# Kernel optimization log

Measured on AMD Instinct MI355X. Metric: run time of the kernel, lower is better.

## Reference

```python
import jax, jax.numpy as jnp
import numpy as np

BN_EPS = 1e-5


def _bn(x, gamma, beta):
    # BatchNorm2d in training mode: batch statistics over (B, T, V) per channel.
    mean = jnp.mean(x, axis=(0, 2, 3), keepdims=True)
    var = jnp.var(x, axis=(0, 2, 3), keepdims=True)
    inv = jax.lax.rsqrt(var + BN_EPS)
    g = gamma[None, :, None, None]
    b = beta[None, :, None, None]
    return (x - mean) * inv * g + b


def setup_inputs() -> dict:
    key = jax.random.key(0)
    ks = jax.random.split(key, 8)
    B, Cin, Cout, T, V = 32, 64, 128, 300, 25
    x = jax.random.normal(ks[0], (B, Cin, T, V), dtype=jnp.float32)
    A_hat = jax.random.uniform(ks[1], (V, V), dtype=jnp.float32) / V  # row-normalized-ish adjacency
    # spatial 1x1 conv weight/bias
    w_sp = jax.random.normal(ks[2], (Cout, Cin), dtype=jnp.float32) * (1.0 / np.sqrt(Cin))
    b_sp = jnp.zeros((Cout,), dtype=jnp.float32)
    g_sp = jnp.ones((Cout,), dtype=jnp.float32)
    be_sp = jnp.zeros((Cout,), dtype=jnp.float32)
    # temporal conv (9,1) weight/bias, same channels
    w_t = jax.random.normal(ks[3], (Cout, Cout, 9, 1), dtype=jnp.float32) * (1.0 / np.sqrt(Cout * 9))
    b_t = jnp.zeros((Cout,), dtype=jnp.float32)
    g_t = jnp.ones((Cout,), dtype=jnp.float32)
    be_t = jnp.zeros((Cout,), dtype=jnp.float32)
    # residual 1x1 conv + BN (in_channels != out_channels)
    w_r = jax.random.normal(ks[4], (Cout, Cin), dtype=jnp.float32) * (1.0 / np.sqrt(Cin))
    b_r = jnp.zeros((Cout,), dtype=jnp.float32)
    g_r = jnp.ones((Cout,), dtype=jnp.float32)
    be_r = jnp.zeros((Cout,), dtype=jnp.float32)
    return {
        "x": x, "A_hat": A_hat,
        "w_sp": w_sp, "b_sp": b_sp, "g_sp": g_sp, "be_sp": be_sp,
        "w_t": w_t, "b_t": b_t, "g_t": g_t, "be_t": be_t,
        "w_r": w_r, "b_r": b_r, "g_r": g_r, "be_r": be_r,
    }


def reference(x, A_hat, w_sp, b_sp, g_sp, be_sp, w_t, b_t, g_t, be_t, w_r, b_r, g_r, be_r):
    # residual branch: 1x1 conv + BN
    res = jnp.einsum('oc,bctv->botv', w_r, x) + b_r[None, :, None, None]
    res = _bn(res, g_r, be_r)
    # spatial graph conv: A_hat @ x over node dim, then 1x1 conv
    h = jnp.einsum('vw,bctw->bctv', A_hat, x)
    h = jnp.einsum('oc,bctv->botv', w_sp, h) + b_sp[None, :, None, None]
    h = jax.nn.relu(_bn(h, g_sp, be_sp))
    # temporal conv (9,1) with padding (4,0), then BN
    h = jax.lax.conv_general_dilated(
        h, w_t, window_strides=(1, 1), padding=((4, 4), (0, 0)),
        dimension_numbers=('NCHW', 'OIHW', 'NCHW'))
    h = h + b_t[None, :, None, None]
    h = _bn(h, g_t, be_t)
    return jax.nn.relu(h + res)
```

## Files before the change

### kernel.cpp

```cpp
#include <hip/hip_runtime.h>

constexpr int B    = 32;
constexpr int CIN  = 64;
constexpr int COUT = 128;
constexpr int T    = 300;
constexpr int V    = 25;
constexpr int TV   = T * V;
constexpr long long NPC   = (long long)B * TV;
constexpr long long TOTAL = (long long)B * COUT * TV;

typedef short          bf16x8 __attribute__((ext_vector_type(8)));
typedef float          f32x4  __attribute__((ext_vector_type(4)));
typedef unsigned short us8    __attribute__((ext_vector_type(8)));
typedef unsigned short us4    __attribute__((ext_vector_type(4)));

static __device__ __forceinline__ unsigned short f2bf(float f) {
  union { float f; unsigned u; } x; x.f = f;
  unsigned r = x.u + 0x7FFFu + ((x.u >> 16) & 1u);
  return (unsigned short)(r >> 16);
}
static __device__ __forceinline__ float bf2f(unsigned short u) {
  union { unsigned u; float f; } x; x.u = ((unsigned)u) << 16;
  return x.f;
}
static __device__ __forceinline__ unsigned cvtpk(float a, float b) {
  unsigned r;
  asm("v_cvt_pk_bf16_f32 %0, %1, %2" : "=v"(r) : "v"(a), "v"(b));
  return r;
}

static __device__ __forceinline__ int xoff(int pos, int c) {
  return pos * 64 + ((((c >> 3)) ^ (pos & 7)) << 3) + (c & 7);
}
static __device__ __forceinline__ int soff(int c, int pw) {
  return c * 128 + ((((pw >> 3)) ^ (c & 7)) << 3) + (pw & 7);
}

__global__ __launch_bounds__(256) void kPrep(
    const float* __restrict__ w_t, const float* __restrict__ w_r,
    const float* __restrict__ w_sp, const float* __restrict__ A_hat,
    unsigned short* __restrict__ wb2, unsigned short* __restrict__ wrs2,
    unsigned short* __restrict__ bdt)
{
  int i = blockIdx.x * 256 + threadIdx.x;
  if (i < 147456) {
    int c = i & 127, ok = i >> 7;
    int k = ok % 9, o = ok / 9;
    int idx = ((k * 16 + (c >> 3)) * 128 + o) * 8 + (c & 7);
    wb2[idx] = f2bf(w_t[(o * COUT + c) * 9 + k]);
  } else if (i < 147456 + 16384) {
    int j = i - 147456;
    int c = j & 63, row = j >> 6;
    float v = (row < COUT) ? w_r[row * CIN + c] : w_sp[(row - COUT) * CIN + c];
    wrs2[((c >> 3) * 256 + row) * 8 + (c & 7)] = f2bf(v);
  } else {
    int j = i - 147456 - 16384;
    int pv = j >> 7, pw = j & 127;
    float v = 0.f;
    if (pv < 100 && pw < 100 && (pv / 25) == (pw / 25))
      v = A_hat[(pv % 25) * 25 + (pw % 25)];
    bdt[j] = f2bf(v);
  }
}

__global__ __launch_bounds__(256, 3) void kA8(
    const float* __restrict__ x, const unsigned short* __restrict__ bdt,
    const unsigned short* __restrict__ wrs2,
    unsigned short* __restrict__ resb, unsigned short* __restrict__ h,
    float2* __restrict__ part_rs)
{
  __shared__ unsigned short buf[64 * 128];

  const int tid  = threadIdx.x;
  const int lane = tid & 63;
  const int wave = tid >> 6;
  const int b    = blockIdx.y;
  const int p0   = blockIdx.x * 100;
  const int z    = blockIdx.z;
  const int grp  = lane >> 4;
  const int l15  = lane & 15;

  f32x4 acc[2][7];
#pragma unroll
  for (int m = 0; m < 2; ++m)
#pragma unroll
    for (int n = 0; n < 7; ++n) acc[m][n] = (f32x4)0.f;

  const unsigned short* bsrc = buf;

  if (z == 0) {
    for (int u = tid; u < 16 * 112; u += 256) {
      int pos = u % 112, c4 = u / 112;
      int c0 = c4 * 4;
      float v0 = 0.f, v1 = 0.f, v2 = 0.f, v3 = 0.f;
      if (pos < 100) {
        const float* xp = &x[(b * CIN + c0) * TV + p0 + pos];
        v0 = xp[0]; v1 = xp[TV]; v2 = xp[2 * TV]; v3 = xp[3 * TV];
      }
      uint2 w;
      w.x = cvtpk(v0, v1);
      w.y = cvtpk(v2, v3);
      *(uint2*)&buf[xoff(pos, c0)] = w;
    }
    __syncthreads();
  } else {
    for (int u = tid; u < 64 * 32; u += 256) {
      int q = u & 31, c = u >> 5;
      int pos = q * 4;
      float4 v = make_float4(0.f, 0.f, 0.f, 0.f);
      if (pos < 100)
        v = *(const float4*)&x[(b * CIN + c) * TV + p0 + pos];
      us4 pk;
      unsigned u01 = cvtpk(v.x, v.y), u23 = cvtpk(v.z, v.w);
      pk[0] = (unsigned short)u01;
      pk[1] = (unsigned short)(u01 >> 16);
      pk[2] = (unsigned short)u23;
      pk[3] = (unsigned short)(u23 >> 16);
      *(us4*)&buf[soff(c, pos)] = pk;
    }
    __syncthreads();

    bf16x8 xf[4];
#pragma unroll
    for (int ks = 0; ks < 4; ++ks)
      xf[ks] = *(const bf16x8*)&buf[soff(wave * 16 + l15, ks * 32 + grp * 8)];
    __syncthreads();

    {
      f32x4 macc[7];
#pragma unroll
      for (int ni = 0; ni < 7; ++ni) macc[ni] = (f32x4)0.f;
      const int kst[7] = {0, 0, 0, 0, 1, 2, 2};
      const int kcn[7] = {1, 2, 2, 3, 3, 2, 2};
#pragma unroll
      for (int ni = 0; ni < 7; ++ni) {
        for (int kk = 0; kk < kcn[ni]; ++kk) {
          int ks = kst[ni] + kk;
          bf16x8 gf = *(const bf16x8*)&bdt[(ni * 16 + l15) * 128 + ks * 32 + grp * 8];
          macc[ni] = __builtin_amdgcn_mfma_f32_16x16x32_bf16(xf[ks], gf, macc[ni], 0, 0, 0);
        }
      }
      unsigned short* axsp = (unsigned short*)buf;
#pragma unroll
      for (int ni = 0; ni < 7; ++ni) {
#pragma unroll
        for (int r = 0; r < 4; ++r)
          axsp[xoff(ni * 16 + l15, wave * 16 + grp * 4 + r)] = f2bf(macc[ni][r]);
      }
    }
    __syncthreads();
  }

#pragma unroll
  for (int ks = 0; ks < 2; ++ks) {
    bf16x8 af[2], bfr[7];
#pragma unroll
    for (int mi = 0; mi < 2; ++mi) {
      int row = z * 128 + wave * 32 + mi * 16 + l15;
      af[mi] = *(const bf16x8*)&wrs2[((ks * 4 + grp) * 256 + row) * 8];
    }
#pragma unroll
    for (int ni = 0; ni < 7; ++ni)
      bfr[ni] = *(const bf16x8*)&bsrc[xoff(ni * 16 + l15, ks * 32 + grp * 8)];
#pragma unroll
    for (int mi = 0; mi < 2; ++mi)
#pragma unroll
      for (int ni = 0; ni < 7; ++ni)
        acc[mi][ni] = __builtin_amdgcn_mfma_f32_16x16x32_bf16(
            af[mi], bfr[ni], acc[mi][ni], 0, 0, 0);
  }

  if (z == 0) {
#pragma unroll
    for (int mi = 0; mi < 2; ++mi) {
#pragma unroll
      for (int ni = 0; ni < 7; ++ni) {
        int pos = ni * 16 + l15;
        if (pos < 100) {
#pragma unroll
          for (int r = 0; r < 4; ++r) {
            int c = wave * 32 + mi * 16 + grp * 4 + r;
            resb[((long long)(b * COUT + c)) * TV + p0 + pos] = f2bf(acc[mi][ni][r]);
          }
        }
      }
    }
  } else {
#pragma unroll
    for (int mi = 0; mi < 2; ++mi) {
      int o0 = wave * 32 + mi * 16 + grp * 4;
#pragma unroll
      for (int ni = 0; ni < 7; ++ni) {
        int pos = ni * 16 + l15;
        if (pos < 100) {
          uint2 w;
          w.x = cvtpk(acc[mi][ni][0], acc[mi][ni][1]);
          w.y = cvtpk(acc[mi][ni][2], acc[mi][ni][3]);
          *(uint2*)&h[((long long)(b * TV + p0 + pos)) * COUT + o0] = w;
        }
      }
    }
  }

  {
    float sv[8], qv[8];
#pragma unroll
    for (int mi = 0; mi < 2; ++mi)
#pragma unroll
      for (int r = 0; r < 4; ++r) {
        float s = 0.f, q = 0.f;
#pragma unroll
        for (int ni = 0; ni < 7; ++ni) {
          float v = (ni < 6 || l15 < 4) ? acc[mi][ni][r] : 0.f;
          s += v; q += v * v;
        }
        sv[mi * 4 + r] = s; qv[mi * 4 + r] = q;
      }
#pragma unroll
    for (int bm = 1; bm < 8; bm <<= 1) {
      const bool up = (l15 & bm) != 0;
#pragma unroll
      for (int i = 0; i < 8; i += 2 * bm) {
        const int j = i + bm;
        float ssend = up ? sv[i] : sv[j];
        float qsend = up ? qv[i] : qv[j];
        float sgot = __shfl_xor(ssend, bm);
        float qgot = __shfl_xor(qsend, bm);
        sv[i] = (up ? sv[j] : sv[i]) + sgot;
        qv[i] = (up ? qv[j] : qv[i]) + qgot;
      }
    }
    sv[0] += __shfl_xor(sv[0], 8);
    qv[0] += __shfl_xor(qv[0], 8);
    if ((l15 & 8) == 0) {
      int slot = ((l15 >> 2) * 16) + grp * 4 + (l15 & 3);
      float2* pw = &part_rs[((((long long)(blockIdx.y * 75 + blockIdx.x)) * 2 + z) * 4 + wave) * 32];
      pw[slot] = make_float2(sv[0], qv[0]);
    }
  }
}

__global__ __launch_bounds__(256) void kC2v2(
    const float2* __restrict__ part_rs,
    const float* __restrict__ g_r,  const float* __restrict__ be_r,
    const float* __restrict__ g_sp, const float* __restrict__ be_sp,
    float* __restrict__ scales)
{
  __shared__ float rs[256], rq[256];
  const int row = blockIdx.x;
  const int z = row >> 7, wave = (row >> 5) & 3, slot = row & 31;
  const int tid = threadIdx.x;
  float s = 0.f, q = 0.f;
  for (int bid = tid; bid < 2400; bid += 256) {
    float2 v = part_rs[(((long long)bid * 2 + z) * 4 + wave) * 32 + slot];
    s += v.x; q += v.y;
  }
  rs[tid] = s; rq[tid] = q;
  __syncthreads();
  for (int st = 128; st > 0; st >>= 1) {
    if (tid < st) { rs[tid] += rs[tid + st]; rq[tid] += rq[tid + st]; }
    __syncthreads();
  }
  if (tid == 0) {
    const float n = (float)NPC;
    float m = rs[0] / n, var = rq[0] / n - m * m;
    float iv = rsqrtf(var + 1e-5f);
    if (row < 128) {
      float sc = g_r[row] * iv;
      scales[row] = sc; scales[128 + row] = be_r[row] - m * sc;
    } else {
      int c = row - 128;
      float sc = g_sp[c] * iv;
      scales[256 + c] = sc; scales[384 + c] = be_sp[c] - m * sc;
    }
  }
}

constexpr int NP    = 256;
constexpr int HALO  = 100;
constexpr int STAGE = NP + 2 * HALO;

__global__ __launch_bounds__(512, 2) void kE7d(
    const unsigned short* __restrict__ h, const unsigned short* __restrict__ wb2,
    const float* __restrict__ scales, unsigned short* __restrict__ cvb,
    float2* __restrict__ part_t)
{
  __shared__ unsigned short hs[STAGE * 64];
  const int tid  = threadIdx.x;
  const int lane = tid & 63;
  const int wave = tid >> 6;
  const int wm   = wave >> 2, wn = wave & 3;
  const int b    = blockIdx.y;
  const int p0   = blockIdx.x * NP;
  const int grp  = lane >> 4;
  const int l15  = lane & 15;
  const int slot = tid & 7;

  f32x4 acc[4][4];
#pragma unroll
  for (int m = 0; m < 4; ++m)
#pragma unroll
    for (int n = 0; n < 4; ++n) acc[m][n] = (f32x4)0.f;

  for (int cc = 0; cc < 2; ++cc) {
    if (cc) __syncthreads();
    const int c0 = cc * 64;
    float sc[8], sh[8];
#pragma unroll
    for (int e = 0; e < 8; ++e) {
      sc[e] = scales[256 + c0 + slot * 8 + e];
      sh[e] = scales[384 + c0 + slot * 8 + e];
    }
    for (int i = tid; i < STAGE * 8; i += 512) {
      int pos = i >> 3;
      int pg = p0 - HALO + pos;
      uint4 w = {0u, 0u, 0u, 0u};
      if (pg >= 0 && pg < TV) {
        us8 v = *(const us8*)&h[((long long)b * TV + pg) * COUT + c0 + slot * 8];
        float f[8];
#pragma unroll
        for (int e = 0; e < 8; ++e)
          f[e] = fmaxf(bf2f(v[e]) * sc[e] + sh[e], 0.f);
        w.x = cvtpk(f[0], f[1]);
        w.y = cvtpk(f[2], f[3]);
        w.z = cvtpk(f[4], f[5]);
        w.w = cvtpk(f[6], f[7]);
      }
      int si = (pos << 6) + ((slot ^ (pos & 7)) << 3);
      *(uint4*)&hs[si] = w;
    }
    __syncthreads();

    __builtin_amdgcn_s_setprio(1);
    for (int k = 0; k < 9; ++k) {
      const int plb = HALO + wn * 64 + 25 * (k - 4) + l15;
#pragma unroll
      for (int ks = 0; ks < 2; ++ks) {
        bf16x8 af[4], bfr[4];
#pragma unroll
        for (int mi = 0; mi < 4; ++mi) {
          int o = wm * 64 + mi * 16 + l15;
          af[mi] = *(const bf16x8*)&wb2[((k * 16 + cc * 8 + ks * 4 + grp) * 128 + o) * 8];
        }
#pragma unroll
        for (int ni = 0; ni < 4; ++ni) {
          int pl = plb + ni * 16;
          int si = (pl << 6) + (((ks * 4 + grp) ^ (pl & 7)) << 3);
          bfr[ni] = *(const bf16x8*)&hs[si];
        }
#pragma unroll
        for (int mi = 0; mi < 4; ++mi)
#pragma unroll
          for (int ni = 0; ni < 4; ++ni)
            acc[mi][ni] = __builtin_amdgcn_mfma_f32_16x16x32_bf16(
                af[mi], bfr[ni], acc[mi][ni], 0, 0, 0);
      }
    }
    __builtin_amdgcn_s_setprio(0);
  }

#pragma unroll
  for (int mi = 0; mi < 4; ++mi) {
#pragma unroll
    for (int ni = 0; ni < 4; ++ni) {
      int pos = p0 + wn * 64 + ni * 16 + l15;
      if (pos < TV) {
#pragma unroll
        for (int r = 0; r < 4; ++r) {
          int o = wm * 64 + mi * 16 + grp * 4 + r;
          cvb[((long long)(b * COUT + o)) * TV + pos] = f2bf(acc[mi][ni][r]);
        }
      }
    }
  }

  {
    float sv[16], qv[16];
#pragma unroll
    for (int mi = 0; mi < 4; ++mi)
#pragma unroll
      for (int r = 0; r < 4; ++r) {
        float s = 0.f, q = 0.f;
#pragma unroll
        for (int ni = 0; ni < 4; ++ni) {
          int pos = p0 + wn * 64 + ni * 16 + l15;
          float v = (pos < TV) ? acc[mi][ni][r] : 0.f;
          s += v; q += v * v;
        }
        sv[mi * 4 + r] = s; qv[mi * 4 + r] = q;
      }
#pragma unroll
    for (int bm = 1; bm < 16; bm <<= 1) {
      const bool up = (l15 & bm) != 0;
#pragma unroll
      for (int i = 0; i < 16; i += 2 * bm) {
        const int j = i + bm;
        float ssend = up ? sv[i] : sv[j];
        float qsend = up ? qv[i] : qv[j];
        float sgot = __shfl_xor(ssend, bm);
        float qgot = __shfl_xor(qsend, bm);
        sv[i] = (up ? sv[j] : sv[i]) + sgot;
        qv[i] = (up ? qv[j] : qv[i]) + qgot;
      }
    }
    int slt = ((l15 >> 2) * 16) + grp * 4 + (l15 & 3);
    float2* pw = &part_t[(((long long)(blockIdx.y * 30 + blockIdx.x)) * 8 + wave) * 64];
    pw[slt] = make_float2(sv[0], qv[0]);
  }
}

__global__ __launch_bounds__(256) void kG2(
    const float2* __restrict__ part_t,
    const float* __restrict__ g_t, const float* __restrict__ be_t,
    float* __restrict__ scales)
{
  __shared__ float rs[256], rq[256];
  const int c = blockIdx.x;
  const int wm = c >> 6, local = c & 63;
  const int tid = threadIdx.x;
  const int NB = 30 * 32;
  float s = 0.f, q = 0.f;
  for (int p = tid; p < NB * 4; p += 256) {
    int bid = p >> 2, wn = p & 3;
    float2 v = part_t[((long long)bid * 8 + (wm * 4 + wn)) * 64 + local];
    s += v.x; q += v.y;
  }
  rs[tid] = s; rq[tid] = q;
  __syncthreads();
  for (int st = 128; st > 0; st >>= 1) {
    if (tid < st) { rs[tid] += rs[tid + st]; rq[tid] += rq[tid + st]; }
    __syncthreads();
  }
  if (tid == 0) {
    const float n = (float)NPC;
    float m = rs[0] / n, var = rq[0] / n - m * m;
    float sc = g_t[c] * rsqrtf(var + 1e-5f);
    scales[512 + c] = sc;
    scales[640 + c] = be_t[c] - m * sc;
  }
}

__global__ __launch_bounds__(256) void kH(
    const unsigned short* __restrict__ cvb, const unsigned short* __restrict__ resb,
    const float* __restrict__ scales, float* __restrict__ out)
{
  const int plane = blockIdx.x;
  const int c = plane & 127;
  const float sct = scales[512 + c], sht = scales[640 + c];
  const float scr = scales[c],       shr = scales[128 + c];
  const us4* cp = (const us4*)&cvb[(long long)plane * TV];
  const us4* rp = (const us4*)&resb[(long long)plane * TV];
  float* op = &out[(long long)plane * TV];
  for (int u = threadIdx.x; u < 1875; u += 256) {
    us4 o4 = cp[u], r4 = rp[u];
    float4 y;
    y.x = fmaxf(bf2f(o4[0]) * sct + sht + bf2f(r4[0]) * scr + shr, 0.f);
    y.y = fmaxf(bf2f(o4[1]) * sct + sht + bf2f(r4[1]) * scr + shr, 0.f);
    y.z = fmaxf(bf2f(o4[2]) * sct + sht + bf2f(r4[2]) * scr + shr, 0.f);
    y.w = fmaxf(bf2f(o4[3]) * sct + sht + bf2f(r4[3]) * scr + shr, 0.f);
    *(float4*)&op[u * 4] = y;
  }
}

extern "C" void kernel_launch(void* const* d_in, const int* in_sizes, int n_in,
                              void* d_out, int out_size, void* d_ws, size_t ws_size,
                              hipStream_t stream) {
  const float* x     = (const float*)d_in[0];
  const float* A_hat = (const float*)d_in[1];
  const float* w_sp  = (const float*)d_in[2];
  const float* g_sp  = (const float*)d_in[4];
  const float* be_sp = (const float*)d_in[5];
  const float* w_t   = (const float*)d_in[6];
  const float* g_t   = (const float*)d_in[8];
  const float* be_t  = (const float*)d_in[9];
  const float* w_r   = (const float*)d_in[10];
  const float* g_r   = (const float*)d_in[12];
  const float* be_r  = (const float*)d_in[13];
  float* out = (float*)d_out;

  unsigned short* base_us = (unsigned short*)d_ws;
  unsigned short* resb = base_us;
  unsigned short* h    = base_us + (size_t)TOTAL;
  unsigned short* cvb  = base_us + (size_t)(2 * TOTAL);
  unsigned short* wb2  = base_us + (size_t)(3 * TOTAL);
  unsigned short* wrs2 = wb2 + 147456;
  unsigned short* bdt  = wrs2 + 16384;
  float2* part_rs = (float2*)(bdt + 14336);
  float2* part_t  = part_rs + 2400 * 2 * 4 * 32;
  float*  scales  = (float*)(part_t + 960 * 8 * 64);

  kPrep<<<696, 256, 0, stream>>>(w_t, w_r, w_sp, A_hat, wb2, wrs2, bdt);
  kA8<<<dim3(75, 32, 2), 256, 0, stream>>>(x, bdt, wrs2, resb, h, part_rs);
  kC2v2<<<256, 256, 0, stream>>>(part_rs, g_r, be_r, g_sp, be_sp, scales);
  kE7d<<<dim3(30, 32), 512, 0, stream>>>(h, wb2, scales, cvb, part_t);
  kG2<<<128, 256, 0, stream>>>(part_t, g_t, be_t, scales);
  kH<<<4096, 256, 0, stream>>>(cvb, resb, scales, out);
}
```

Before: 225.6 us.

## Merge residual and spatial branches into one block sharing the x tile

Kernel A previously launched two z-slices per tile: one computed the residual 1x1 conv and the other computed the graph conv plus the spatial 1x1 conv, and each slice loaded x from global memory separately. The new kernel does both branches in a single block, staging x into two shared-memory layouts and running the two GEMMs one after the other. This halves the grid and drops the duplicated launch-level work. In exchange it doubles shared memory per block and serialises the two branches, which may lower occupancy and the parallelism available to each block. The x tile is still read from global memory twice, once for each layout.

Measured after the change: 233.4 us. 1.03x slower.

```diff
diff --git a/kernel.cpp b/kernel.cpp
--- a/kernel.cpp
+++ b/kernel.cpp
@@ -63,105 +63,70 @@
   }
 }
 
-__global__ __launch_bounds__(256, 3) void kA8(
+__global__ __launch_bounds__(256, 3) void kA9(
     const float* __restrict__ x, const unsigned short* __restrict__ bdt,
     const unsigned short* __restrict__ wrs2,
     unsigned short* __restrict__ resb, unsigned short* __restrict__ h,
     float2* __restrict__ part_rs)
 {
-  __shared__ unsigned short buf[64 * 128];
+  __shared__ unsigned short xs[64 * 128];
+  __shared__ unsigned short xsp[112 * 64];
 
   const int tid  = threadIdx.x;
   const int lane = tid & 63;
   const int wave = tid >> 6;
   const int b    = blockIdx.y;
   const int p0   = blockIdx.x * 100;
-  const int z    = blockIdx.z;
   const int grp  = lane >> 4;
   const int l15  = lane & 15;
+  const long long bid2 = ((long long)(blockIdx.y * 75 + blockIdx.x)) * 2;
+
+  for (int u = tid; u < 64 * 32; u += 256) {
+    int q = u & 31, c = u >> 5;
+    int pos = q * 4;
+    float4 v = make_float4(0.f, 0.f, 0.f, 0.f);
+    if (pos < 100)
+      v = *(const float4*)&x[(b * CIN + c) * TV + p0 + pos];
+    us4 pk;
+    unsigned u01 = cvtpk(v.x, v.y), u23 = cvtpk(v.z, v.w);
+    pk[0] = (unsigned short)u01;
+    pk[1] = (unsigned short)(u01 >> 16);
+    pk[2] = (unsigned short)u23;
+    pk[3] = (unsigned short)(u23 >> 16);
+    *(us4*)&xs[soff(c, pos)] = pk;
+  }
+  for (int u = tid; u < 16 * 112; u += 256) {
+    int pos = u % 112, c4 = u / 112;
+    int c0 = c4 * 4;
+    float v0 = 0.f, v1 = 0.f, v2 = 0.f, v3 = 0.f;
+    if (pos < 100) {
+      const float* xp = &x[(b * CIN + c0) * TV + p0 + pos];
+      v0 = xp[0]; v1 = xp[TV]; v2 = xp[2 * TV]; v3 = xp[3 * TV];
+    }
+    uint2 w;
+    w.x = cvtpk(v0, v1);
+    w.y = cvtpk(v2, v3);
+    *(uint2*)&xsp[xoff(pos, c0)] = w;
+  }
+  __syncthreads();
 
   f32x4 acc[2][7];
 #pragma unroll
   for (int m = 0; m < 2; ++m)
 #pragma unroll
     for (int n = 0; n < 7; ++n) acc[m][n] = (f32x4)0.f;
-
-  const unsigned short* bsrc = buf;
-
-  if (z == 0) {
-    for (int u = tid; u < 16 * 112; u += 256) {
-      int pos = u % 112, c4 = u / 112;
-      int c0 = c4 * 4;
-      float v0 = 0.f, v1 = 0.f, v2 = 0.f, v3 = 0.f;
-      if (pos < 100) {
-        const float* xp = &x[(b * CIN + c0) * TV + p0 + pos];
-        v0 = xp[0]; v1 = xp[TV]; v2 = xp[2 * TV]; v3 = xp[3 * TV];
-      }
-      uint2 w;
-      w.x = cvtpk(v0, v1);
-      w.y = cvtpk(v2, v3);
-      *(uint2*)&buf[xoff(pos, c0)] = w;
-    }
-    __syncthreads();
-  } else {
-    for (int u = tid; u < 64 * 32; u += 256) {
-      int q = u & 31, c = u >> 5;
-      int pos = q * 4;
-      float4 v = make_float4(0.f, 0.f, 0.f, 0.f);
-      if (pos < 100)
-        v = *(const float4*)&x[(b * CIN + c) * TV + p0 + pos];
-      us4 pk;
-      unsigned u01 = cvtpk(v.x, v.y), u23 = cvtpk(v.z, v.w);
-      pk[0] = (unsigned short)u01;
-      pk[1] = (unsigned short)(u01 >> 16);
-      pk[2] = (unsigned short)u23;
-      pk[3] = (unsigned short)(u23 >> 16);
-      *(us4*)&buf[soff(c, pos)] = pk;
-    }
-    __syncthreads();
-
-    bf16x8 xf[4];
-#pragma unroll
-    for (int ks = 0; ks < 4; ++ks)
-      xf[ks] = *(const bf16x8*)&buf[soff(wave * 16 + l15, ks * 32 + grp * 8)];
-    __syncthreads();
-
-    {
-      f32x4 macc[7];
-#pragma unroll
-      for (int ni = 0; ni < 7; ++ni) macc[ni] = (f32x4)0.f;
-      const int kst[7] = {0, 0, 0, 0, 1, 2, 2};
-      const int kcn[7] = {1, 2, 2, 3, 3, 2, 2};
-#pragma unroll
-      for (int ni = 0; ni < 7; ++ni) {
-        for (int kk = 0; kk < kcn[ni]; ++kk) {
-          int ks = kst[ni] + kk;
-          bf16x8 gf = *(const bf16x8*)&bdt[(ni * 16 + l15) * 128 + ks * 32 + grp * 8];
-          macc[ni] = __builtin_amdgcn_mfma_f32_16x16x32_bf16(xf[ks], gf, macc[ni], 0, 0, 0);
-        }
-      }
-      unsigned short* axsp = (unsigned short*)buf;
-#pragma unroll
-      for (int ni = 0; ni < 7; ++ni) {
-#pragma unroll
-        for (int r = 0; r < 4; ++r)
-          axsp[xoff(ni * 16 + l15, wave * 16 + grp * 4 + r)] = f2bf(macc[ni][r]);
-      }
-    }
-    __syncthreads();
-  }
 
 #pragma unroll
   for (int ks = 0; ks < 2; ++ks) {
     bf16x8 af[2], bfr[7];
 #pragma unroll
     for (int mi = 0; mi < 2; ++mi) {
-      int row = z * 128 + wave * 32 + mi * 16 + l15;
+      int row = wave * 32 + mi * 16 + l15;
       af[mi] = *(const bf16x8*)&wrs2[((ks * 4 + grp) * 256 + row) * 8];
     }
 #pragma unroll
     for (int ni = 0; ni < 7; ++ni)
-      bfr[ni] = *(const bf16x8*)&bsrc[xoff(ni * 16 + l15, ks * 32 + grp * 8)];
+      bfr[ni] = *(const bf16x8*)&xsp[xoff(ni * 16 + l15, ks * 32 + grp * 8)];
 #pragma unroll
     for (int mi = 0; mi < 2; ++mi)
 #pragma unroll
@@ -169,39 +134,20 @@
         acc[mi][ni] = __builtin_amdgcn_mfma_f32_16x16x32_bf16(
             af[mi], bfr[ni], acc[mi][ni], 0, 0, 0);
   }
-
-  if (z == 0) {
-#pragma unroll
-    for (int mi = 0; mi < 2; ++mi) {
-#pragma unroll
-      for (int ni = 0; ni < 7; ++ni) {
-        int pos = ni * 16 + l15;
-        if (pos < 100) {
-#pragma unroll
-          for (int r = 0; r < 4; ++r) {
-            int c = wave * 32 + mi * 16 + grp * 4 + r;
-            resb[((long long)(b * COUT + c)) * TV + p0 + pos] = f2bf(acc[mi][ni][r]);
-          }
-        }
-      }
-    }
-  } else {
-#pragma unroll
-    for (int mi = 0; mi < 2; ++mi) {
-      int o0 = wave * 32 + mi * 16 + grp * 4;
-#pragma unroll
-      for (int ni = 0; ni < 7; ++ni) {
-        int pos = ni * 16 + l15;
-        if (pos < 100) {
-          uint2 w;
-          w.x = cvtpk(acc[mi][ni][0], acc[mi][ni][1]);
-          w.y = cvtpk(acc[mi][ni][2], acc[mi][ni][3]);
-          *(uint2*)&h[((long long)(b * TV + p0 + pos)) * COUT + o0] = w;
-        }
-      }
-    }
-  }
-
+#pragma unroll
+  for (int mi = 0; mi < 2; ++mi) {
+#pragma unroll
+    for (int ni = 0; ni < 7; ++ni) {
+      int pos = ni * 16 + l15;
+      if (pos < 100) {
+#pragma unroll
+        for (int r = 0; r < 4; ++r) {
+          int c = wave * 32 + mi * 16 + grp * 4 + r;
+          resb[((long long)(b * COUT + c)) * TV + p0 + pos] = f2bf(acc[mi][ni][r]);
+        }
+      }
+    }
+  }
   {
     float sv[8], qv[8];
 #pragma unroll
@@ -234,8 +180,111 @@
     qv[0] += __shfl_xor(qv[0], 8);
     if ((l15 & 8) == 0) {
       int slot = ((l15 >> 2) * 16) + grp * 4 + (l15 & 3);
-      float2* pw = &part_rs[((((long long)(blockIdx.y * 75 + blockIdx.x)) * 2 + z) * 4 + wave) * 32];
-      pw[slot] = make_float2(sv[0], qv[0]);
+      part_rs[((bid2 + 0) * 4 + wave) * 32 + slot] = make_float2(sv[0], qv[0]);
+    }
+  }
+
+  bf16x8 xf[4];
+#pragma unroll
+  for (int ks = 0; ks < 4; ++ks)
+    xf[ks] = *(const bf16x8*)&xs[soff(wave * 16 + l15, ks * 32 + grp * 8)];
+  __syncthreads();
+
+  {
+    f32x4 macc[7];
+#pragma unroll
+    for (int ni = 0; ni < 7; ++ni) macc[ni] = (f32x4)0.f;
+    const int kst[7] = {0, 0, 0, 0, 1, 2, 2};
+    const int kcn[7] = {1, 2, 2, 3, 3, 2, 2};
+#pragma unroll
+    for (int ni = 0; ni < 7; ++ni) {
+      for (int kk = 0; kk < kcn[ni]; ++kk) {
+        int ks = kst[ni] + kk;
+        bf16x8 gf = *(const bf16x8*)&bdt[(ni * 16 + l15) * 128 + ks * 32 + grp * 8];
+        macc[ni] = __builtin_amdgcn_mfma_f32_16x16x32_bf16(xf[ks], gf, macc[ni], 0, 0, 0);
+      }
+    }
+    unsigned short* axsp = (unsigned short*)xs;
+#pragma unroll
+    for (int ni = 0; ni < 7; ++ni) {
+#pragma unroll
+      for (int r = 0; r < 4; ++r)
+        axsp[xoff(ni * 16 + l15, wave * 16 + grp * 4 + r)] = f2bf(macc[ni][r]);
+    }
+  }
+  __syncthreads();
+
+#pragma unroll
+  for (int m = 0; m < 2; ++m)
+#pragma unroll
+    for (int n = 0; n < 7; ++n) acc[m][n] = (f32x4)0.f;
+
+  const unsigned short* axsp = xs;
+#pragma unroll
+  for (int ks = 0; ks < 2; ++ks) {
+    bf16x8 af[2], bfr[7];
+#pragma unroll
+    for (int mi = 0; mi < 2; ++mi) {
+      int row = 128 + wave * 32 + mi * 16 + l15;
+      af[mi] = *(const bf16x8*)&wrs2[((ks * 4 + grp) * 256 + row) * 8];
+    }
+#pragma unroll
+    for (int ni = 0; ni < 7; ++ni)
+      bfr[ni] = *(const bf16x8*)&axsp[xoff(ni * 16 + l15, ks * 32 + grp * 8)];
+#pragma unroll
+    for (int mi = 0; mi < 2; ++mi)
+#pragma unroll
+      for (int ni = 0; ni < 7; ++ni)
+        acc[mi][ni] = __builtin_amdgcn_mfma_f32_16x16x32_bf16(
+            af[mi], bfr[ni], acc[mi][ni], 0, 0, 0);
+  }
+#pragma unroll
+  for (int mi = 0; mi < 2; ++mi) {
+    int o0 = wave * 32 + mi * 16 + grp * 4;
+#pragma unroll
+    for (int ni = 0; ni < 7; ++ni) {
+      int pos = ni * 16 + l15;
+      if (pos < 100) {
+        uint2 w;
+        w.x = cvtpk(acc[mi][ni][0], acc[mi][ni][1]);
+        w.y = cvtpk(acc[mi][ni][2], acc[mi][ni][3]);
+        *(uint2*)&h[((long long)(b * TV + p0 + pos)) * COUT + o0] = w;
+      }
+    }
+  }
+  {
+    float sv[8], qv[8];
+#pragma unroll
+    for (int mi = 0; mi < 2; ++mi)
+#pragma unroll
+      for (int r = 0; r < 4; ++r) {
+        float s = 0.f, q = 0.f;
+#pragma unroll
+        for (int ni = 0; ni < 7; ++ni) {
+          float v = (ni < 6 || l15 < 4) ? acc[mi][ni][r] : 0.f;
+          s += v; q += v * v;
+        }
+        sv[mi * 4 + r] = s; qv[mi * 4 + r] = q;
+      }
+#pragma unroll
+    for (int bm = 1; bm < 8; bm <<= 1) {
+      const bool up = (l15 & bm) != 0;
+#pragma unroll
+      for (int i = 0; i < 8; i += 2 * bm) {
+        const int j = i + bm;
+        float ssend = up ? sv[i] : sv[j];
+        float qsend = up ? qv[i] : qv[j];
+        float sgot = __shfl_xor(ssend, bm);
+        float qgot = __shfl_xor(qsend, bm);
+        sv[i] = (up ? sv[j] : sv[i]) + sgot;
+        qv[i] = (up ? qv[j] : qv[i]) + qgot;
+      }
+    }
+    sv[0] += __shfl_xor(sv[0], 8);
+    qv[0] += __shfl_xor(qv[0], 8);
+    if ((l15 & 8) == 0) {
+      int slot = ((l15 >> 2) * 16) + grp * 4 + (l15 & 3);
+      part_rs[((bid2 + 1) * 4 + wave) * 32 + slot] = make_float2(sv[0], qv[0]);
     }
   }
 }
@@ -490,7 +539,7 @@
   float*  scales  = (float*)(part_t + 960 * 8 * 64);
 
   kPrep<<<696, 256, 0, stream>>>(w_t, w_r, w_sp, A_hat, wb2, wrs2, bdt);
-  kA8<<<dim3(75, 32, 2), 256, 0, stream>>>(x, bdt, wrs2, resb, h, part_rs);
+  kA9<<<dim3(75, 32), 256, 0, stream>>>(x, bdt, wrs2, resb, h, part_rs);
   kC2v2<<<256, 256, 0, stream>>>(part_rs, g_r, be_r, g_sp, be_sp, scales);
   kE7d<<<dim3(30, 32), 512, 0, stream>>>(h, wb2, scales, cvb, part_t);
   kG2<<<128, 256, 0, stream>>>(part_t, g_t, be_t, scales);
```
